# Performance work log

Hardware: AMD Instinct MI355X
Metric: run time of the kernel (lower is better)

Reference implementation:

```python
import jax, jax.numpy as jnp
import numpy as np

EPS = 1e-8  # torch F.cosine_similarity eps


def _l2norm(x):
    # x / max(||x||, eps), matching torch cosine_similarity's clamped denominator
    n = jnp.sqrt(jnp.sum(x * x, axis=-1, keepdims=True))
    return x / jnp.maximum(n, EPS)


def setup_inputs() -> dict:
    key = jax.random.key(0)
    k1, k2, k3 = jax.random.split(key, 3)
    B, S, C, D = 16, 512, 16, 512
    return {
        "output": jax.random.normal(k1, (B, C), dtype=jnp.float32),
        "target_text_feats": jax.random.normal(k2, (B, S, C, D), dtype=jnp.float32),
        "vis_feats": jax.random.normal(k3, (B, S, D), dtype=jnp.float32),
    }


def reference(output, target_text_feats, vis_feats):
    B, S, C, D = target_text_feats.shape
    vn = _l2norm(vis_feats)              # (B, S, D)
    tn = _l2norm(target_text_feats)      # (B, S, C, D)
    # sim[b,p,v,t] = cos(vis[b,v], text[b,t,p]); replaces the per-prompt python loop
    sim = jnp.einsum('bvd,btpd->bpvt', vn, tn)  # (B, C, S, S)
    diag = jnp.diagonal(sim, axis1=-2, axis2=-1)      # (B, C, S): sim[b,p,i,i]
    lse_row = jax.nn.logsumexp(sim, axis=-1)          # CE over text axis (logits_per_image)
    lse_col = jax.nn.logsumexp(sim, axis=-2)          # CE over vis axis  (logits_per_text)
    # per-sample clip loss, averaged over the v axis -> (B, C)
    clip_loss = jnp.mean(0.5 * (lse_row + lse_col) - diag, axis=-1)
    clip_loss = jax.lax.stop_gradient(clip_loss)      # computed under torch.no_grad()

    loss = jnp.mean(jnp.square(output - clip_loss))

    gt_labels = jnp.argmin(clip_loss, axis=-1)        # (B,)
    preds = jnp.argmin(output, axis=-1)               # (B,)
    acc = jnp.mean((preds == gt_labels).astype(jnp.float32)) * 100.0
    prompt_id_preds = jnp.broadcast_to(preds[:, None, None], (B, S, 1))
    return loss, acc, prompt_id_preds
```

## Files before the change

kernel.cpp:

```cpp
#include <hip/hip_runtime.h>

#define EPSN 1e-8f

typedef _Float16 half8 __attribute__((ext_vector_type(8)));
typedef float floatx4 __attribute__((ext_vector_type(4)));

__global__ __launch_bounds__(256) void k_vinv(const float* __restrict__ vis,
                                              float* __restrict__ vinv) {
    int row  = blockIdx.x * 4 + (threadIdx.x >> 6);
    int lane = threadIdx.x & 63;
    const float4* src = reinterpret_cast<const float4*>(vis + (size_t)row * 512);
    float4 a = src[lane];
    float4 b = src[lane + 64];
    float s = a.x*a.x + a.y*a.y + a.z*a.z + a.w*a.w
            + b.x*b.x + b.y*b.y + b.z*b.z + b.w*b.w;
    #pragma unroll
    for (int off = 1; off < 64; off <<= 1) s += __shfl_xor(s, off);
    if (lane == 0) vinv[row] = 1.0f / fmaxf(sqrtf(s), EPSN);
}

#define LDA 40
#define LDB 40

__global__ __launch_bounds__(512, 2) void k_main(
    const float* __restrict__ vis, const float* __restrict__ text,
    const float* __restrict__ vinv,
    float* __restrict__ g_rowsum, float* __restrict__ g_colsum,
    float* __restrict__ g_dsum)
{
    __shared__ _Float16 Ash[512 * LDA];
    __shared__ _Float16 Bsh[128 * LDB];
    __shared__ float tn2[128];
    __shared__ float colS[128];

    const int blk  = blockIdx.x;
    const int tb   = blk & 3;
    const int p    = (blk >> 2) & 15;
    const int b    = blk >> 6;
    const int bp   = blk >> 2;
    const int tid  = threadIdx.x;
    const int lane = tid & 63;
    const int wave = tid >> 6;
    const int t0   = tb * 128;
    const int m15  = lane & 15;
    const int g4   = lane >> 4;

    if (tid < 128) { tn2[tid] = 0.f; colS[tid] = 0.f; }
    __syncthreads();

    floatx4 acc[4][8];
    floatx4 zf = {0.f, 0.f, 0.f, 0.f};
    #pragma unroll
    for (int mb = 0; mb < 4; ++mb)
        #pragma unroll
        for (int nb = 0; nb < 8; ++nb) acc[mb][nb] = zf;

    const float* visB = vis + (size_t)b * 512 * 512;
    const int brow = tid >> 2;
    const int bko  = (tid & 3) * 8;
    const float* textRow =
        text + ((size_t)((b * 512 + t0 + brow) * 16 + p)) * 512;

    for (int kc = 0; kc < 16; ++kc) {
        const int k0 = kc * 32;
        #pragma unroll
        for (int c = 0; c < 4; ++c) {
            int g   = c * 512 + tid;
            int row = g >> 2;
            int ko  = (g & 3) * 8;
            const float4* s4 =
                reinterpret_cast<const float4*>(visB + (size_t)row * 512 + k0 + ko);
            float4 f0 = s4[0], f1 = s4[1];
            half8 h = { (_Float16)f0.x, (_Float16)f0.y, (_Float16)f0.z, (_Float16)f0.w,
                        (_Float16)f1.x, (_Float16)f1.y, (_Float16)f1.z, (_Float16)f1.w };
            *reinterpret_cast<half8*>(&Ash[row * LDA + ko]) = h;
        }
        {
            const float4* s4 = reinterpret_cast<const float4*>(textRow + k0 + bko);
            float4 f0 = s4[0], f1 = s4[1];
            float sq = f0.x*f0.x + f0.y*f0.y + f0.z*f0.z + f0.w*f0.w
                     + f1.x*f1.x + f1.y*f1.y + f1.z*f1.z + f1.w*f1.w;
            sq += __shfl_xor(sq, 1);
            sq += __shfl_xor(sq, 2);
            if ((lane & 3) == 0) atomicAdd(&tn2[brow], sq);
            half8 h = { (_Float16)f0.x, (_Float16)f0.y, (_Float16)f0.z, (_Float16)f0.w,
                        (_Float16)f1.x, (_Float16)f1.y, (_Float16)f1.z, (_Float16)f1.w };
            *reinterpret_cast<half8*>(&Bsh[brow * LDB + bko]) = h;
        }
        __syncthreads();
        half8 af[4];
        #pragma unroll
        for (int mb = 0; mb < 4; ++mb)
            af[mb] = *reinterpret_cast<const half8*>(
                &Ash[(wave * 64 + mb * 16 + m15) * LDA + g4 * 8]);
        #pragma unroll
        for (int nb = 0; nb < 8; ++nb) {
            half8 bf = *reinterpret_cast<const half8*>(
                &Bsh[(nb * 16 + m15) * LDB + g4 * 8]);
            #pragma unroll
            for (int mb = 0; mb < 4; ++mb)
                acc[mb][nb] = __builtin_amdgcn_mfma_f32_16x16x32_f16(
                    af[mb], bf, acc[mb][nb], 0, 0, 0);
        }
        __syncthreads();
    }

    if (tid < 128) tn2[tid] = 1.0f / fmaxf(sqrtf(tn2[tid]), EPSN);
    __syncthreads();

    float tinvc[8];
    #pragma unroll
    for (int nb = 0; nb < 8; ++nb) tinvc[nb] = tn2[nb * 16 + m15];

    float colpart[8];
    #pragma unroll
    for (int nb = 0; nb < 8; ++nb) colpart[nb] = 0.f;
    float dsum = 0.f;

    #pragma unroll
    for (int mb = 0; mb < 4; ++mb) {
        #pragma unroll
        for (int r = 0; r < 4; ++r) {
            int vglob = wave * 64 + mb * 16 + g4 * 4 + r;
            float vi  = vinv[b * 512 + vglob];
            float rp  = 0.f;
            #pragma unroll
            for (int nb = 0; nb < 8; ++nb) {
                float sim  = acc[mb][nb][r] * vi * tinvc[nb];
                int tglob  = t0 + nb * 16 + m15;
                if (vglob == tglob) dsum += sim;
                float e = __expf(sim);
                rp += e;
                colpart[nb] += e;
            }
            rp += __shfl_xor(rp, 1);
            rp += __shfl_xor(rp, 2);
            rp += __shfl_xor(rp, 4);
            rp += __shfl_xor(rp, 8);
            if (m15 == 0)
                atomicAdd(&g_rowsum[(size_t)bp * 512 + vglob], rp);
        }
    }
    #pragma unroll
    for (int nb = 0; nb < 8; ++nb) {
        float cp = colpart[nb];
        cp += __shfl_xor(cp, 16);
        cp += __shfl_xor(cp, 32);
        if (lane < 16) atomicAdd(&colS[nb * 16 + lane], cp);
    }
    #pragma unroll
    for (int off = 1; off < 64; off <<= 1) dsum += __shfl_xor(dsum, off);
    if (lane == 0) atomicAdd(&g_dsum[bp], dsum);
    __syncthreads();
    if (tid < 128)
        g_colsum[(size_t)bp * 512 + t0 + tid] = colS[tid];
}

__global__ __launch_bounds__(256) void k_clip(
    const float* __restrict__ g_rowsum, const float* __restrict__ g_colsum,
    const float* __restrict__ g_dsum, float* __restrict__ clip)
{
    __shared__ float red[4];
    int bp = blockIdx.x, tid = threadIdx.x;
    int lane = tid & 63, wave = tid >> 6;
    float s = 0.f;
    #pragma unroll
    for (int c = 0; c < 2; ++c) {
        int i = c * 256 + tid;
        s += 0.5f * (logf(g_rowsum[(size_t)bp * 512 + i]) +
                     logf(g_colsum[(size_t)bp * 512 + i]));
    }
    #pragma unroll
    for (int off = 1; off < 64; off <<= 1) s += __shfl_xor(s, off);
    if (lane == 0) red[wave] = s;
    __syncthreads();
    if (tid == 0)
        clip[bp] = (red[0] + red[1] + red[2] + red[3] - g_dsum[bp]) * (1.0f / 512.0f);
}

__global__ __launch_bounds__(256) void k_final(
    const float* __restrict__ clip, const float* __restrict__ output,
    float* __restrict__ out)
{
    __shared__ float cl[256], ou[256], red[4];
    __shared__ int preds[16];
    int tid = threadIdx.x, lane = tid & 63, wave = tid >> 6;
    cl[tid] = clip[tid];
    ou[tid] = output[tid];
    __syncthreads();
    float d = ou[tid] - cl[tid];
    float s = d * d;
    #pragma unroll
    for (int off = 1; off < 64; off <<= 1) s += __shfl_xor(s, off);
    if (lane == 0) red[wave] = s;
    if (tid < 16) {
        float m = ou[tid * 16]; int a = 0;
        for (int q = 1; q < 16; ++q)
            if (ou[tid * 16 + q] < m) { m = ou[tid * 16 + q]; a = q; }
        preds[tid] = a;
    }
    __syncthreads();
    if (tid == 0) {
        int cnt = 0;
        for (int bb = 0; bb < 16; ++bb) {
            float m = cl[bb * 16]; int a = 0;
            for (int q = 1; q < 16; ++q)
                if (cl[bb * 16 + q] < m) { m = cl[bb * 16 + q]; a = q; }
            cnt += (preds[bb] == a);
        }
        out[0] = (red[0] + red[1] + red[2] + red[3]) * (1.0f / 256.0f);
        out[1] = (float)cnt * (100.0f / 16.0f);
    }
    __syncthreads();
    for (int j = tid; j < 16 * 512; j += 256)
        out[2 + j] = (float)preds[j >> 9];
}

extern "C" void kernel_launch(void* const* d_in, const int* in_sizes, int n_in,
                              void* d_out, int out_size, void* d_ws, size_t ws_size,
                              hipStream_t stream)
{
    const float* output = (const float*)d_in[0];
    const float* text   = (const float*)d_in[1];
    const float* vis    = (const float*)d_in[2];

    float* g_rowsum = (float*)d_ws;
    float* g_dsum   = g_rowsum + 256 * 512;
    float* g_colsum = g_dsum + 256;
    float* clip     = g_colsum + 256 * 512;
    float* vinv     = clip + 256;
    hipMemsetAsync(d_ws, 0, (size_t)(256 * 512 + 256) * sizeof(float), stream);

    k_vinv <<<2048, 256, 0, stream>>>(vis, vinv);
    k_main <<<1024, 512, 0, stream>>>(vis, text, vinv, g_rowsum, g_colsum, g_dsum);
    k_clip <<<256, 256, 0, stream>>>(g_rowsum, g_colsum, g_dsum, clip);
    k_final<<<1, 256, 0, stream>>>(clip, output, (float*)d_out);
}
```

Before: 552.2 us.

## Split main GEMM blocks along vis rows and accumulate text norms in registers

Each main block now covers half of the vis rows (256 instead of 512) using 256 threads, which doubles the grid to 2048 blocks and halves the A tile in shared memory. Column sums are now added atomically into global memory, and the memset grows to zero them. Text squared norms are summed in per-thread registers and reduced once after the K loop, replacing the per-chunk LDS atomics. The split means each text tile is loaded and converted twice, and the extra global atomics add traffic.

```diff
diff --git a/kernel.cpp b/kernel.cpp
--- a/kernel.cpp
+++ b/kernel.cpp
@@ -22,31 +22,32 @@
 #define LDA 40
 #define LDB 40
 
-__global__ __launch_bounds__(512, 2) void k_main(
+__global__ __launch_bounds__(256, 2) void k_main(
     const float* __restrict__ vis, const float* __restrict__ text,
     const float* __restrict__ vinv,
     float* __restrict__ g_rowsum, float* __restrict__ g_colsum,
     float* __restrict__ g_dsum)
 {
-    __shared__ _Float16 Ash[512 * LDA];
+    __shared__ _Float16 Ash[256 * LDA];
     __shared__ _Float16 Bsh[128 * LDB];
     __shared__ float tn2[128];
     __shared__ float colS[128];
 
     const int blk  = blockIdx.x;
-    const int tb   = blk & 3;
-    const int p    = (blk >> 2) & 15;
-    const int b    = blk >> 6;
-    const int bp   = blk >> 2;
+    const int vh   = blk & 1;
+    const int tb   = (blk >> 1) & 3;
+    const int bp   = blk >> 3;
+    const int p    = bp & 15;
+    const int b    = bp >> 4;
     const int tid  = threadIdx.x;
     const int lane = tid & 63;
     const int wave = tid >> 6;
+    const int v0   = vh * 256;
     const int t0   = tb * 128;
     const int m15  = lane & 15;
     const int g4   = lane >> 4;
 
-    if (tid < 128) { tn2[tid] = 0.f; colS[tid] = 0.f; }
-    __syncthreads();
+    if (tid < 128) colS[tid] = 0.f;
 
     floatx4 acc[4][8];
     floatx4 zf = {0.f, 0.f, 0.f, 0.f};
@@ -55,37 +56,48 @@
         #pragma unroll
         for (int nb = 0; nb < 8; ++nb) acc[mb][nb] = zf;
 
-    const float* visB = vis + (size_t)b * 512 * 512;
-    const int brow = tid >> 2;
+    const float* visB = vis + (size_t)b * 512 * 512 + (size_t)v0 * 512;
+    const int arow = tid >> 2;
+    const int ako  = (tid & 3) * 8;
+    const int brow0 = tid >> 2;
+    const int brow1 = 64 + (tid >> 2);
     const int bko  = (tid & 3) * 8;
-    const float* textRow =
-        text + ((size_t)((b * 512 + t0 + brow) * 16 + p)) * 512;
+    const float* textRow0 =
+        text + ((size_t)((b * 512 + t0 + brow0) * 16 + p)) * 512;
+    const float* textRow1 =
+        text + ((size_t)((b * 512 + t0 + brow1) * 16 + p)) * 512;
+
+    float sq0 = 0.f, sq1 = 0.f;
 
     for (int kc = 0; kc < 16; ++kc) {
         const int k0 = kc * 32;
         #pragma unroll
         for (int c = 0; c < 4; ++c) {
-            int g   = c * 512 + tid;
-            int row = g >> 2;
-            int ko  = (g & 3) * 8;
+            int row = c * 64 + arow;
             const float4* s4 =
-                reinterpret_cast<const float4*>(visB + (size_t)row * 512 + k0 + ko);
+                reinterpret_cast<const float4*>(visB + (size_t)row * 512 + k0 + ako);
             float4 f0 = s4[0], f1 = s4[1];
             half8 h = { (_Float16)f0.x, (_Float16)f0.y, (_Float16)f0.z, (_Float16)f0.w,
                         (_Float16)f1.x, (_Float16)f1.y, (_Float16)f1.z, (_Float16)f1.w };
-            *reinterpret_cast<half8*>(&Ash[row * LDA + ko]) = h;
+            *reinterpret_cast<half8*>(&Ash[row * LDA + ako]) = h;
         }
         {
-            const float4* s4 = reinterpret_cast<const float4*>(textRow + k0 + bko);
+            const float4* s4 = reinterpret_cast<const float4*>(textRow0 + k0 + bko);
             float4 f0 = s4[0], f1 = s4[1];
-            float sq = f0.x*f0.x + f0.y*f0.y + f0.z*f0.z + f0.w*f0.w
-                     + f1.x*f1.x + f1.y*f1.y + f1.z*f1.z + f1.w*f1.w;
-            sq += __shfl_xor(sq, 1);
-            sq += __shfl_xor(sq, 2);
-            if ((lane & 3) == 0) atomicAdd(&tn2[brow], sq);
+            sq0 += f0.x*f0.x + f0.y*f0.y + f0.z*f0.z + f0.w*f0.w
+                 + f1.x*f1.x + f1.y*f1.y + f1.z*f1.z + f1.w*f1.w;
             half8 h = { (_Float16)f0.x, (_Float16)f0.y, (_Float16)f0.z, (_Float16)f0.w,
                         (_Float16)f1.x, (_Float16)f1.y, (_Float16)f1.z, (_Float16)f1.w };
-            *reinterpret_cast<half8*>(&Bsh[brow * LDB + bko]) = h;
+            *reinterpret_cast<half8*>(&Bsh[brow0 * LDB + bko]) = h;
+        }
+        {
+            const float4* s4 = reinterpret_cast<const float4*>(textRow1 + k0 + bko);
+            float4 f0 = s4[0], f1 = s4[1];
+            sq1 += f0.x*f0.x + f0.y*f0.y + f0.z*f0.z + f0.w*f0.w
+                 + f1.x*f1.x + f1.y*f1.y + f1.z*f1.z + f1.w*f1.w;
+            half8 h = { (_Float16)f0.x, (_Float16)f0.y, (_Float16)f0.z, (_Float16)f0.w,
+                        (_Float16)f1.x, (_Float16)f1.y, (_Float16)f1.z, (_Float16)f1.w };
+            *reinterpret_cast<half8*>(&Bsh[brow1 * LDB + bko]) = h;
         }
         __syncthreads();
         half8 af[4];
@@ -105,7 +117,12 @@
         __syncthreads();
     }
 
-    if (tid < 128) tn2[tid] = 1.0f / fmaxf(sqrtf(tn2[tid]), EPSN);
+    sq0 += __shfl_xor(sq0, 1); sq0 += __shfl_xor(sq0, 2);
+    sq1 += __shfl_xor(sq1, 1); sq1 += __shfl_xor(sq1, 2);
+    if ((tid & 3) == 0) {
+        tn2[brow0] = 1.0f / fmaxf(sqrtf(sq0), EPSN);
+        tn2[brow1] = 1.0f / fmaxf(sqrtf(sq1), EPSN);
+    }
     __syncthreads();
 
     float tinvc[8];
@@ -121,7 +138,7 @@
     for (int mb = 0; mb < 4; ++mb) {
         #pragma unroll
         for (int r = 0; r < 4; ++r) {
-            int vglob = wave * 64 + mb * 16 + g4 * 4 + r;
+            int vglob = v0 + wave * 64 + mb * 16 + g4 * 4 + r;
             float vi  = vinv[b * 512 + vglob];
             float rp  = 0.f;
             #pragma unroll
@@ -153,7 +170,7 @@
     if (lane == 0) atomicAdd(&g_dsum[bp], dsum);
     __syncthreads();
     if (tid < 128)
-        g_colsum[(size_t)bp * 512 + t0 + tid] = colS[tid];
+        atomicAdd(&g_colsum[(size_t)bp * 512 + t0 + tid], colS[tid]);
 }
 
 __global__ __launch_bounds__(256) void k_clip(
@@ -225,14 +242,14 @@
     const float* vis    = (const float*)d_in[2];
 
     float* g_rowsum = (float*)d_ws;
-    float* g_dsum   = g_rowsum + 256 * 512;
-    float* g_colsum = g_dsum + 256;
-    float* clip     = g_colsum + 256 * 512;
+    float* g_colsum = g_rowsum + 256 * 512;
+    float* g_dsum   = g_colsum + 256 * 512;
+    float* clip     = g_dsum + 256;
     float* vinv     = clip + 256;
-    hipMemsetAsync(d_ws, 0, (size_t)(256 * 512 + 256) * sizeof(float), stream);
+    hipMemsetAsync(d_ws, 0, (size_t)(2 * 256 * 512 + 256) * sizeof(float), stream);
 
     k_vinv <<<2048, 256, 0, stream>>>(vis, vinv);
-    k_main <<<1024, 512, 0, stream>>>(vis, text, vinv, g_rowsum, g_colsum, g_dsum);
+    k_main <<<2048, 256, 0, stream>>>(vis, text, vinv, g_rowsum, g_colsum, g_dsum);
     k_clip <<<256, 256, 0, stream>>>(g_rowsum, g_colsum, g_dsum, clip);
     k_final<<<1, 256, 0, stream>>>(clip, output, (float*)d_out);
 }
```

Result: faster. 482.6 us (-12.6%).
